# Kernel optimization log

Hardware: AMD Instinct MI355X
Metric: run time of the kernel (lower is better)

## Reference

```python
import jax, jax.numpy as jnp
import numpy as np

INPUT_DELAY_SIZE = 32
OUTPUT_DELAY_SIZE = 64
INPUT_SIZE = 64
OUTPUT_SIZE = 1
BATCH = 16384
DI = INPUT_DELAY_SIZE * INPUT_SIZE      # 2048
DO = OUTPUT_DELAY_SIZE * OUTPUT_SIZE    # 64


def setup_inputs() -> dict:
    key = jax.random.key(0)
    k1, k2, k3, k4, k5, k6 = jax.random.split(key, 6)
    return {
        "input": jax.random.normal(k1, (BATCH, INPUT_SIZE), dtype=jnp.float32),
        "itdl": jax.random.normal(k2, (BATCH, DI, 1), dtype=jnp.float32),
        "otdl": jax.random.normal(k3, (BATCH, DO, 1), dtype=jnp.float32),
        "iw": 0.01 * jax.random.normal(k4, (1, DI), dtype=jnp.float32),
        "ow": 0.01 * jax.random.normal(k5, (1, DO), dtype=jnp.float32),
        "b": 0.01 * jax.random.normal(k6, (1, 1), dtype=jnp.float32),
    }


def reference(input, itdl, otdl, iw, ow, b):
    # __pred: zero_input_delay=False -> delay = itdl
    # [1,DI] @ [B,DI,1] -> [B,1,1]; [1,DO] @ [B,DO,1] -> [B,1,1]
    a2 = jnp.matmul(iw, itdl) + jnp.matmul(ow, otdl) + b  # [B,1,1]
    # insert_tdl: shift register -- drop oldest `shift` taps, append new sample
    itdl_new = jnp.concatenate(
        [itdl[:, INPUT_SIZE:, :], input.reshape(-1, INPUT_SIZE, 1)], axis=1
    )
    otdl_new = jnp.concatenate([otdl[:, OUTPUT_SIZE:, :], a2], axis=1)
    outputs = a2.reshape(-1, 1, OUTPUT_SIZE)
    return outputs, itdl_new, otdl_new
```

## Files before the change

kernel.cpp:

```cpp
#include <hip/hip_runtime.h>

#define BATCH 16384
#define DI 2048
#define DO 64
#define IS 64

__global__ __launch_bounds__(256) void arx_cell_kernel(
    const float* __restrict__ input,
    const float* __restrict__ itdl,
    const float* __restrict__ otdl,
    const float* __restrict__ iw,
    const float* __restrict__ ow,
    const float* __restrict__ bias,
    float* __restrict__ out)
{
    const int b = blockIdx.x;
    const int t = threadIdx.x;

    const float* it = itdl + (size_t)b * DI;
    float* out0 = out;
    float* out1 = out + BATCH;
    float* out2 = out + BATCH + (size_t)BATCH * DI;

    const int k0 = t * 8;
    float4 v0 = *(const float4*)(it + k0);
    float4 v1 = *(const float4*)(it + k0 + 4);
    float4 w0 = *(const float4*)(iw + k0);
    float4 w1 = *(const float4*)(iw + k0 + 4);
    float partial = v0.x * w0.x + v0.y * w0.y + v0.z * w0.z + v0.w * w0.w
                  + v1.x * w1.x + v1.y * w1.y + v1.z * w1.z + v1.w * w1.w;

    float oval = 0.0f;
    if (t < DO) {
        oval = otdl[(size_t)b * DO + t];
        partial += oval * ow[t];
    }

    float* o1 = out1 + (size_t)b * DI;
    if (k0 >= IS) {
        *(float4*)(o1 + (k0 - IS))     = v0;
        *(float4*)(o1 + (k0 - IS) + 4) = v1;
    } else {
        const float* in = input + (size_t)b * IS;
        float4 i0 = *(const float4*)(in + k0);
        float4 i1 = *(const float4*)(in + k0 + 4);
        *(float4*)(o1 + (DI - IS) + k0)     = i0;
        *(float4*)(o1 + (DI - IS) + k0 + 4) = i1;
    }

    if (t >= 1 && t < DO) {
        out2[(size_t)b * DO + (t - 1)] = oval;
    }

    #pragma unroll
    for (int off = 32; off > 0; off >>= 1)
        partial += __shfl_down(partial, off, 64);

    __shared__ float sred[4];
    if ((t & 63) == 0) sred[t >> 6] = partial;
    __syncthreads();

    if (t == 0) {
        float a2 = sred[0] + sred[1] + sred[2] + sred[3] + bias[0];
        out0[b] = a2;
        out2[(size_t)b * DO + (DO - 1)] = a2;
    }
}

extern "C" void kernel_launch(void* const* d_in, const int* in_sizes, int n_in,
                              void* d_out, int out_size, void* d_ws, size_t ws_size,
                              hipStream_t stream) {
    const float* input = (const float*)d_in[0];
    const float* itdl  = (const float*)d_in[1];
    const float* otdl  = (const float*)d_in[2];
    const float* iw    = (const float*)d_in[3];
    const float* ow    = (const float*)d_in[4];
    const float* bias  = (const float*)d_in[5];
    float* out = (float*)d_out;

    arx_cell_kernel<<<BATCH, 256, 0, stream>>>(input, itdl, otdl, iw, ow, bias, out);
}
```

Before: 246.6 us.

## Map one wavefront per batch row and drop block-level reduction

Each 64-lane wavefront now handles a whole batch row, with 8 coalesced float4 loads per lane, instead of one 256-thread block per row. The reduction becomes a single wave shuffle, so the shared-memory step and __syncthreads are gone, and the grid shrinks by four. The aim is less per-block overhead and more bytes in flight per thread in this bandwidth-bound copy-plus-dot kernel. The cost is more registers per thread.

```diff
diff --git a/kernel.cpp b/kernel.cpp
--- a/kernel.cpp
+++ b/kernel.cpp
@@ -14,56 +14,60 @@
     const float* __restrict__ bias,
     float* __restrict__ out)
 {
-    const int b = blockIdx.x;
-    const int t = threadIdx.x;
+    const int t    = threadIdx.x;
+    const int lane = t & 63;
+    const int row  = blockIdx.x * 4 + (t >> 6);
 
-    const float* it = itdl + (size_t)b * DI;
+    const float* it = itdl + (size_t)row * DI;
     float* out0 = out;
-    float* out1 = out + BATCH;
-    float* out2 = out + BATCH + (size_t)BATCH * DI;
+    float* o1   = out + BATCH + (size_t)row * DI;
+    float* o2   = out + BATCH + (size_t)BATCH * DI
+                      + (size_t)row * DO;
 
-    const int k0 = t * 8;
-    float4 v0 = *(const float4*)(it + k0);
-    float4 v1 = *(const float4*)(it + k0 + 4);
-    float4 w0 = *(const float4*)(iw + k0);
-    float4 w1 = *(const float4*)(iw + k0 + 4);
-    float partial = v0.x * w0.x + v0.y * w0.y + v0.z * w0.z + v0.w * w0.w
-                  + v1.x * w1.x + v1.y * w1.y + v1.z * w1.z + v1.w * w1.w;
+    float4 v[8];
+    #pragma unroll
+    for (int j = 0; j < 8; ++j)
+        v[j] = *(const float4*)(it + j * 256 + lane * 4);
 
-    float oval = 0.0f;
-    if (t < DO) {
-        oval = otdl[(size_t)b * DO + t];
-        partial += oval * ow[t];
+    float4 in0 = make_float4(0.f, 0.f, 0.f, 0.f);
+    if (lane < 16)
+        in0 = *(const float4*)(input + (size_t)row * IS + lane * 4);
+
+    float oval = otdl[(size_t)row * DO + lane];
+
+    float partial = 0.f;
+    #pragma unroll
+    for (int j = 0; j < 8; ++j) {
+        float4 wv = *(const float4*)(iw + j * 256 + lane * 4);
+        partial += v[j].x * wv.x + v[j].y * wv.y
+                 + v[j].z * wv.z + v[j].w * wv.w;
+    }
+    partial += oval * ow[lane];
+
+    #pragma unroll
+    for (int j = 0; j < 8; ++j) {
+        const int k = j * 256 + lane * 4;
+        if (j == 0) {
+            if (lane < 16) {
+                *(float4*)(o1 + (DI - IS) + lane * 4) = in0;
+            } else {
+                *(float4*)(o1 + k - IS) = v[j];
+            }
+        } else {
+            *(float4*)(o1 + k - IS) = v[j];
+        }
     }
 
-    float* o1 = out1 + (size_t)b * DI;
-    if (k0 >= IS) {
-        *(float4*)(o1 + (k0 - IS))     = v0;
-        *(float4*)(o1 + (k0 - IS) + 4) = v1;
-    } else {
-        const float* in = input + (size_t)b * IS;
-        float4 i0 = *(const float4*)(in + k0);
-        float4 i1 = *(const float4*)(in + k0 + 4);
-        *(float4*)(o1 + (DI - IS) + k0)     = i0;
-        *(float4*)(o1 + (DI - IS) + k0 + 4) = i1;
-    }
-
-    if (t >= 1 && t < DO) {
-        out2[(size_t)b * DO + (t - 1)] = oval;
-    }
+    if (lane >= 1) o2[lane - 1] = oval;
 
     #pragma unroll
     for (int off = 32; off > 0; off >>= 1)
         partial += __shfl_down(partial, off, 64);
 
-    __shared__ float sred[4];
-    if ((t & 63) == 0) sred[t >> 6] = partial;
-    __syncthreads();
-
-    if (t == 0) {
-        float a2 = sred[0] + sred[1] + sred[2] + sred[3] + bias[0];
-        out0[b] = a2;
-        out2[(size_t)b * DO + (DO - 1)] = a2;
+    if (lane == 0) {
+        float a2 = partial + bias[0];
+        out0[row]    = a2;
+        o2[DO - 1]   = a2;
     }
 }
 
@@ -78,5 +82,5 @@
     const float* bias  = (const float*)d_in[5];
     float* out = (float*)d_out;
 
-    arx_cell_kernel<<<BATCH, 256, 0, stream>>>(input, itdl, otdl, iw, ow, bias, out);
+    arx_cell_kernel<<<BATCH / 4, 256, 0, stream>>>(input, itdl, otdl, iw, ow, bias, out);
 }
```

Result: no change. 250.7 us (+1.7%).
